# Kernel tuning notes

Measured on AMD Instinct MI355X. Metric: run time of the kernel, lower is better.

Reference implementation:

```python
import jax, jax.numpy as jnp
import numpy as np

S, B, C, H = 384, 2, 768, 12
CC = C // H

def setup_inputs() -> dict:
    key = jax.random.key(0)
    ks = jax.random.split(key, 8)
    x = jax.random.normal(ks[0], (S, B, C), dtype=jnp.float32)
    pe = jax.random.normal(ks[1], (S, S, B, C), dtype=jnp.float32)
    # causal mask: True where key index t > query index s (masked out)
    cm = (jnp.arange(S)[None, :] > jnp.arange(S)[:, None])[:, :, None]
    cm = jnp.broadcast_to(cm, (S, S, B))
    pm = jnp.zeros((S, S, B), dtype=bool)  # unused by the module's forward
    stdv = 1.0 / C ** 0.5
    qkv_w = jax.random.normal(ks[2], (3 * C, C), dtype=jnp.float32) * stdv
    qkv_b = jax.random.normal(ks[3], (3 * C,), dtype=jnp.float32) * stdv
    u = jax.random.uniform(ks[4], (C,), minval=-stdv, maxval=stdv, dtype=jnp.float32)
    w = jax.random.uniform(ks[5], (C,), minval=-stdv, maxval=stdv, dtype=jnp.float32)
    out_w = jax.random.normal(ks[6], (C, C), dtype=jnp.float32) * stdv
    out_b = jax.random.normal(ks[7], (C,), dtype=jnp.float32) * stdv
    return {"x": x, "pe": pe, "cm": cm, "pm": pm, "qkv_w": qkv_w,
            "qkv_b": qkv_b, "u": u, "w": w, "out_w": out_w, "out_b": out_b}

def reference(x, pe, cm, pm, qkv_w, qkv_b, u, w, out_w, out_b):
    s, b, c = x.shape
    qkv = x @ qkv_w.T + qkv_b                       # (s,b,3c)
    q, k, v = jnp.split(qkv, 3, axis=-1)
    q = q.reshape(s, b, H, CC)
    k = k.reshape(s, b, H, CC)
    v = v.reshape(s, b, H, CC)
    uh = u.reshape(1, 1, H, CC)
    wh = w.reshape(1, 1, H, CC)
    # content-content scores with global content bias u
    dd_ud = jnp.einsum('sbhc,tbhc->stbh', q + uh, k)
    # content-position scores against dense pairwise pe
    pe5 = pe.reshape(s, s, b, H, CC)
    dp_wp = jnp.einsum('sbhc,stbhc->stbh', q + wh, pe5)
    scale = 1.0 / CC ** 0.5
    a = (dd_ud + dp_wp) * scale
    a = jnp.where(cm[..., None], -jnp.inf, a)       # causal mask (intended)
    p = jax.nn.softmax(a, axis=1)                   # softmax over key axis t
    o = jnp.einsum('stbh,tbhc->sbhc', p, v).reshape(s, b, c)
    return o @ out_w.T + out_b
```

## Files before the change

kernel.cpp:

```cpp
#include <hip/hip_runtime.h>
#include <hip/hip_bf16.h>
#include <cstdint>

constexpr int kS  = 384;
constexpr int kB  = 2;
constexpr int kC  = 768;
constexpr int kH  = 12;
constexpr int kCC = 64;
constexpr int kHPB = 4;

typedef __attribute__((ext_vector_type(8))) short short8;
typedef __attribute__((ext_vector_type(4))) float f32x4;
typedef __attribute__((ext_vector_type(4))) unsigned short u16x4;
typedef const __attribute__((address_space(1))) unsigned int glb_u32_t;
typedef __attribute__((address_space(3))) unsigned int lds_u32_t;

static __device__ __forceinline__ ushort f2bf(float f) {
  __hip_bfloat16 h = __float2bfloat16(f);
  return *reinterpret_cast<ushort*>(&h);
}

__global__ __launch_bounds__(256) void convert_bf16(
    const float* __restrict__ x, const float* __restrict__ qw,
    const float* __restrict__ ow, ushort* __restrict__ xb,
    ushort* __restrict__ qwb, ushort* __restrict__ owb) {
  int idx = blockIdx.x * 256 + threadIdx.x;
  const float* src;
  ushort* dst;
  if (idx < 147456) {
    src = x; dst = xb;
  } else if (idx < 147456 + 442368) {
    idx -= 147456; src = qw; dst = qwb;
  } else {
    idx -= 589824; src = ow; dst = owb;
  }
  f32x4 v = *reinterpret_cast<const f32x4*>(src + (size_t)idx * 4);
  u16x4 o;
  o[0] = f2bf(v[0]); o[1] = f2bf(v[1]); o[2] = f2bf(v[2]); o[3] = f2bf(v[3]);
  *reinterpret_cast<u16x4*>(dst + (size_t)idx * 4) = o;
}

__global__ __launch_bounds__(256) void gemm_bf16_lds(
    const ushort* __restrict__ Abf, const ushort* __restrict__ Wbf,
    const float* __restrict__ bias, float* __restrict__ Cg,
    int M, int N, int K) {
  __shared__ ushort As[64 * 64];
  __shared__ ushort Ws[64 * 64];
  const int tid = threadIdx.x;
  const int m0 = blockIdx.y * 64, n0 = blockIdx.x * 64;
  const int wv = tid >> 6, l = tid & 63;
  const int wr = wv >> 1, wc = wv & 1;
  const int lr = l & 15, lk = l >> 4;

  f32x4 acc[2][2] = {{{0.f, 0.f, 0.f, 0.f}, {0.f, 0.f, 0.f, 0.f}},
                     {{0.f, 0.f, 0.f, 0.f}, {0.f, 0.f, 0.f, 0.f}}};

  for (int k0 = 0; k0 < K; k0 += 64) {
    __syncthreads();
#pragma unroll
    for (int j = 0; j < 2; ++j) {
      int cid = (j * 4 + wv) * 64 + l;
      int r = cid >> 3, c = cid & 7;
      int cs = c ^ (r & 7);
      const ushort* ga = Abf + (size_t)(m0 + r) * K + k0 + cs * 8;
      __builtin_amdgcn_global_load_lds((glb_u32_t*)ga,
                                       (lds_u32_t*)&As[(cid & ~63) * 8],
                                       16, 0, 0);
      const ushort* gw = Wbf + (size_t)(n0 + r) * K + k0 + cs * 8;
      __builtin_amdgcn_global_load_lds((glb_u32_t*)gw,
                                       (lds_u32_t*)&Ws[(cid & ~63) * 8],
                                       16, 0, 0);
    }
    __syncthreads();
#pragma unroll
    for (int ks = 0; ks < 2; ++ks) {
      short8 af[2], bw[2];
#pragma unroll
      for (int f = 0; f < 2; ++f) {
        int ra = wr * 32 + f * 16 + lr;
        int ca = (ks * 4 + lk) ^ (ra & 7);
        af[f] = *reinterpret_cast<const short8*>(&As[(ra * 8 + ca) * 8]);
        int rb = wc * 32 + f * 16 + lr;
        int cb = (ks * 4 + lk) ^ (rb & 7);
        bw[f] = *reinterpret_cast<const short8*>(&Ws[(rb * 8 + cb) * 8]);
      }
#pragma unroll
      for (int fr = 0; fr < 2; ++fr)
#pragma unroll
        for (int fc = 0; fc < 2; ++fc)
          acc[fr][fc] = __builtin_amdgcn_mfma_f32_16x16x32_bf16(
              af[fr], bw[fc], acc[fr][fc], 0, 0, 0);
    }
  }

#pragma unroll
  for (int fr = 0; fr < 2; ++fr)
#pragma unroll
    for (int fc = 0; fc < 2; ++fc)
#pragma unroll
      for (int j = 0; j < 4; ++j) {
        int m = m0 + wr * 32 + fr * 16 + lk * 4 + j;
        int n = n0 + wc * 32 + fc * 16 + lr;
        Cg[(size_t)m * N + n] = acc[fr][fc][j] + bias[n];
      }
}

__global__ __launch_bounds__(256, 6) void attn_kernel(
    const float* __restrict__ qkv, const float* __restrict__ pe,
    const float* __restrict__ u, const float* __restrict__ w,
    ushort* __restrict__ obf) {
  __shared__ float sc[kHPB][kS];

  const int bid = blockIdx.x;
  const int sb = bid / (kH / kHPB);
  const int hg = bid % (kH / kHPB);
  const int s = kS - 1 - (sb >> 1);
  const int b = sb & 1;
  const int wave = threadIdx.x >> 6;
  const int h = hg * kHPB + wave;
  const int lane = threadIdx.x & 63;
  const int tq = lane >> 4;
  const int cq = (lane & 15) * 4;
  const int ch = h * kCC + cq;
  const float scale = 0.125f;

  const int row = s * kB + b;
  const float4 q4 = *(const float4*)&qkv[(int64_t)row * 3 * kC + ch];
  const float4 u4 = *(const float4*)&u[ch];
  const float4 w4 = *(const float4*)&w[ch];
  float4 qu, qw;
  qu.x = q4.x + u4.x; qu.y = q4.y + u4.y; qu.z = q4.z + u4.z; qu.w = q4.w + u4.w;
  qw.x = q4.x + w4.x; qw.y = q4.y + w4.y; qw.z = q4.z + w4.z; qw.w = q4.w + w4.w;

  const float* kbase = qkv + (int64_t)b * 3 * kC + kC + ch;
  const float* vbase = qkv + (int64_t)b * 3 * kC + 2 * kC + ch;
  const float* pbase = pe + ((int64_t)s * kS * kB + b) * kC + ch;
  const int kstride = kB * 3 * kC;
  const int pstride = kB * kC;

  const int nfull = (s + 1) & ~15;

  int t0 = 0;
  for (; t0 < nfull; t0 += 16) {
    float4 k4[4];
    f32x4 p4[4];
#pragma unroll
    for (int i = 0; i < 4; ++i) {
      int t = t0 + i * 4 + tq;
      k4[i] = *(const float4*)&kbase[(int64_t)t * kstride];
      p4[i] = __builtin_nontemporal_load(
          (const f32x4*)&pbase[(int64_t)t * pstride]);
    }
#pragma unroll
    for (int i = 0; i < 4; ++i) {
      float r = qu.x * k4[i].x + qu.y * k4[i].y + qu.z * k4[i].z +
                qu.w * k4[i].w + qw.x * p4[i][0] + qw.y * p4[i][1] +
                qw.z * p4[i][2] + qw.w * p4[i][3];
      r += __shfl_xor(r, 1);
      r += __shfl_xor(r, 2);
      r += __shfl_xor(r, 4);
      r += __shfl_xor(r, 8);
      if ((lane & 15) == 0) sc[wave][t0 + i * 4 + tq] = r * scale;
    }
  }
  for (; t0 <= s; t0 += 4) {
    int t = t0 + tq;
    int tc = (t <= s) ? t : s;
    float4 k4 = *(const float4*)&kbase[(int64_t)tc * kstride];
    float4 p4 = *(const float4*)&pbase[(int64_t)tc * pstride];
    float r = qu.x * k4.x + qu.y * k4.y + qu.z * k4.z + qu.w * k4.w +
              qw.x * p4.x + qw.y * p4.y + qw.z * p4.z + qw.w * p4.w;
    r += __shfl_xor(r, 1);
    r += __shfl_xor(r, 2);
    r += __shfl_xor(r, 4);
    r += __shfl_xor(r, 8);
    if ((lane & 15) == 0 && t <= s) sc[wave][t] = r * scale;
  }
  __syncthreads();

  float mx = -1e30f;
  for (int t = lane; t <= s; t += 64) mx = fmaxf(mx, sc[wave][t]);
#pragma unroll
  for (int off = 32; off; off >>= 1) mx = fmaxf(mx, __shfl_xor(mx, off, 64));
  float sum = 0.f;
  for (int t = lane; t <= s; t += 64) {
    float e = __expf(sc[wave][t] - mx);
    sc[wave][t] = e;
    sum += e;
  }
#pragma unroll
  for (int off = 32; off; off >>= 1) sum += __shfl_xor(sum, off, 64);
  const float rden = 1.0f / sum;

  float4 oa = {0.f, 0.f, 0.f, 0.f};
  t0 = 0;
  for (; t0 < nfull; t0 += 16) {
    float4 v4[4];
    float p[4];
#pragma unroll
    for (int i = 0; i < 4; ++i) {
      int t = t0 + i * 4 + tq;
      v4[i] = *(const float4*)&vbase[(int64_t)t * kstride];
      p[i] = sc[wave][t];
    }
#pragma unroll
    for (int i = 0; i < 4; ++i) {
      oa.x += p[i] * v4[i].x; oa.y += p[i] * v4[i].y;
      oa.z += p[i] * v4[i].z; oa.w += p[i] * v4[i].w;
    }
  }
  for (; t0 <= s; t0 += 4) {
    int t = t0 + tq;
    if (t <= s) {
      float p = sc[wave][t];
      float4 v4 = *(const float4*)&vbase[(int64_t)t * kstride];
      oa.x += p * v4.x; oa.y += p * v4.y; oa.z += p * v4.z; oa.w += p * v4.w;
    }
  }
#pragma unroll
  for (int off = 16; off <= 32; off <<= 1) {
    oa.x += __shfl_xor(oa.x, off);
    oa.y += __shfl_xor(oa.y, off);
    oa.z += __shfl_xor(oa.z, off);
    oa.w += __shfl_xor(oa.w, off);
  }
  if (lane < 16) {
    u16x4 res;
    res[0] = f2bf(oa.x * rden); res[1] = f2bf(oa.y * rden);
    res[2] = f2bf(oa.z * rden); res[3] = f2bf(oa.w * rden);
    *reinterpret_cast<u16x4*>(&obf[(int64_t)row * kC + ch]) = res;
  }
}

extern "C" void kernel_launch(void* const* d_in, const int* in_sizes, int n_in,
                              void* d_out, int out_size, void* d_ws,
                              size_t ws_size, hipStream_t stream) {
  const float* x     = (const float*)d_in[0];
  const float* pe    = (const float*)d_in[1];
  const float* qkv_w = (const float*)d_in[4];
  const float* qkv_b = (const float*)d_in[5];
  const float* u     = (const float*)d_in[6];
  const float* w     = (const float*)d_in[7];
  const float* out_w = (const float*)d_in[8];
  const float* out_b = (const float*)d_in[9];
  float* out = (float*)d_out;

  char* wsb = (char*)d_ws;
  float*  qkv  = (float*)wsb;
  ushort* xb   = (ushort*)(wsb + 7077888);
  ushort* qwb  = (ushort*)(wsb + 8257536);
  ushort* owb  = (ushort*)(wsb + 11796480);
  ushort* obf  = (ushort*)(wsb + 12976128);

  convert_bf16<<<2880, 256, 0, stream>>>(x, qkv_w, out_w, xb, qwb, owb);

  gemm_bf16_lds<<<dim3(3 * kC / 64, kS * kB / 64), 256, 0, stream>>>(
      xb, qwb, qkv_b, qkv, kS * kB, 3 * kC, kC);

  attn_kernel<<<kS * kB * (kH / kHPB), kHPB * 64, 0, stream>>>(
      qkv, pe, u, w, obf);

  gemm_bf16_lds<<<dim3(kC / 64, kS * kB / 64), 256, 0, stream>>>(
      obf, owb, out_b, out, kS * kB, kC, kC);
}
```

Before: 137.2 us.

## Double-buffer GEMM LDS tiles and drop nontemporal pe loads in attention

The GEMM now double-buffers its A and W tiles in LDS, prefetching the next K-slice with global_load_lds while MFMAs run on the current one. It synchronises with a waitcnt plus barrier instead of two syncthreads per iteration. The attention kernel switches pe loads from nontemporal to regular loads, issues them before the k loads, and moves to ext_vector types. The dominant cost is the pe stream in attention, so the GEMM pipelining only touches a smaller part of the runtime, and dropping the nontemporal hint may change cache behaviour.

```diff
diff --git a/kernel.cpp b/kernel.cpp
--- a/kernel.cpp
+++ b/kernel.cpp
@@ -44,8 +44,8 @@
     const ushort* __restrict__ Abf, const ushort* __restrict__ Wbf,
     const float* __restrict__ bias, float* __restrict__ Cg,
     int M, int N, int K) {
-  __shared__ ushort As[64 * 64];
-  __shared__ ushort Ws[64 * 64];
+  __shared__ ushort As[2][64 * 64];
+  __shared__ ushort Ws[2][64 * 64];
   const int tid = threadIdx.x;
   const int m0 = blockIdx.y * 64, n0 = blockIdx.x * 64;
   const int wv = tid >> 6, l = tid & 63;
@@ -55,23 +55,29 @@
   f32x4 acc[2][2] = {{{0.f, 0.f, 0.f, 0.f}, {0.f, 0.f, 0.f, 0.f}},
                      {{0.f, 0.f, 0.f, 0.f}, {0.f, 0.f, 0.f, 0.f}}};
 
-  for (int k0 = 0; k0 < K; k0 += 64) {
-    __syncthreads();
-#pragma unroll
-    for (int j = 0; j < 2; ++j) {
-      int cid = (j * 4 + wv) * 64 + l;
-      int r = cid >> 3, c = cid & 7;
-      int cs = c ^ (r & 7);
-      const ushort* ga = Abf + (size_t)(m0 + r) * K + k0 + cs * 8;
-      __builtin_amdgcn_global_load_lds((glb_u32_t*)ga,
-                                       (lds_u32_t*)&As[(cid & ~63) * 8],
-                                       16, 0, 0);
-      const ushort* gw = Wbf + (size_t)(n0 + r) * K + k0 + cs * 8;
-      __builtin_amdgcn_global_load_lds((glb_u32_t*)gw,
-                                       (lds_u32_t*)&Ws[(cid & ~63) * 8],
-                                       16, 0, 0);
-    }
-    __syncthreads();
+#define STAGE(buf, k0)                                                        \
+  {                                                                           \
+    _Pragma("unroll") for (int j = 0; j < 2; ++j) {                           \
+      int cid = (j * 4 + wv) * 64 + l;                                        \
+      int r = cid >> 3, c = cid & 7;                                          \
+      int cs = c ^ (r & 7);                                                   \
+      __builtin_amdgcn_global_load_lds(                                       \
+          (glb_u32_t*)(Abf + (size_t)(m0 + r) * K + (k0) + cs * 8),           \
+          (lds_u32_t*)&As[buf][(cid & ~63) * 8], 16, 0, 0);                   \
+      __builtin_amdgcn_global_load_lds(                                       \
+          (glb_u32_t*)(Wbf + (size_t)(n0 + r) * K + (k0) + cs * 8),           \
+          (lds_u32_t*)&Ws[buf][(cid & ~63) * 8], 16, 0, 0);                   \
+    }                                                                         \
+  }
+
+  const int NK = K >> 6;
+  STAGE(0, 0);
+  asm volatile("s_waitcnt vmcnt(0)" ::: "memory");
+  __builtin_amdgcn_s_barrier();
+
+  for (int kt = 0; kt < NK; ++kt) {
+    const int cur = kt & 1;
+    if (kt + 1 < NK) STAGE(cur ^ 1, (kt + 1) * 64);
 #pragma unroll
     for (int ks = 0; ks < 2; ++ks) {
       short8 af[2], bw[2];
@@ -79,10 +85,10 @@
       for (int f = 0; f < 2; ++f) {
         int ra = wr * 32 + f * 16 + lr;
         int ca = (ks * 4 + lk) ^ (ra & 7);
-        af[f] = *reinterpret_cast<const short8*>(&As[(ra * 8 + ca) * 8]);
+        af[f] = *reinterpret_cast<const short8*>(&As[cur][(ra * 8 + ca) * 8]);
         int rb = wc * 32 + f * 16 + lr;
         int cb = (ks * 4 + lk) ^ (rb & 7);
-        bw[f] = *reinterpret_cast<const short8*>(&Ws[(rb * 8 + cb) * 8]);
+        bw[f] = *reinterpret_cast<const short8*>(&Ws[cur][(rb * 8 + cb) * 8]);
       }
 #pragma unroll
       for (int fr = 0; fr < 2; ++fr)
@@ -91,7 +97,10 @@
           acc[fr][fc] = __builtin_amdgcn_mfma_f32_16x16x32_bf16(
               af[fr], bw[fc], acc[fr][fc], 0, 0, 0);
     }
-  }
+    asm volatile("s_waitcnt vmcnt(0)" ::: "memory");
+    __builtin_amdgcn_s_barrier();
+  }
+#undef STAGE
 
 #pragma unroll
   for (int fr = 0; fr < 2; ++fr)
@@ -125,12 +134,11 @@
   const float scale = 0.125f;
 
   const int row = s * kB + b;
-  const float4 q4 = *(const float4*)&qkv[(int64_t)row * 3 * kC + ch];
-  const float4 u4 = *(const float4*)&u[ch];
-  const float4 w4 = *(const float4*)&w[ch];
-  float4 qu, qw;
-  qu.x = q4.x + u4.x; qu.y = q4.y + u4.y; qu.z = q4.z + u4.z; qu.w = q4.w + u4.w;
-  qw.x = q4.x + w4.x; qw.y = q4.y + w4.y; qw.z = q4.z + w4.z; qw.w = q4.w + w4.w;
+  const f32x4 q4 = *(const f32x4*)&qkv[(int64_t)row * 3 * kC + ch];
+  const f32x4 u4 = *(const f32x4*)&u[ch];
+  const f32x4 w4 = *(const f32x4*)&w[ch];
+  const f32x4 qu = q4 + u4;
+  const f32x4 qw = q4 + w4;
 
   const float* kbase = qkv + (int64_t)b * 3 * kC + kC + ch;
   const float* vbase = qkv + (int64_t)b * 3 * kC + 2 * kC + ch;
@@ -142,20 +150,22 @@
 
   int t0 = 0;
   for (; t0 < nfull; t0 += 16) {
-    float4 k4[4];
-    f32x4 p4[4];
+    f32x4 k4[4], p4[4];
 #pragma unroll
     for (int i = 0; i < 4; ++i) {
       int t = t0 + i * 4 + tq;
-      k4[i] = *(const float4*)&kbase[(int64_t)t * kstride];
-      p4[i] = __builtin_nontemporal_load(
-          (const f32x4*)&pbase[(int64_t)t * pstride]);
-    }
-#pragma unroll
-    for (int i = 0; i < 4; ++i) {
-      float r = qu.x * k4[i].x + qu.y * k4[i].y + qu.z * k4[i].z +
-                qu.w * k4[i].w + qw.x * p4[i][0] + qw.y * p4[i][1] +
-                qw.z * p4[i][2] + qw.w * p4[i][3];
+      p4[i] = *(const f32x4*)&pbase[(int64_t)t * pstride];
+    }
+#pragma unroll
+    for (int i = 0; i < 4; ++i) {
+      int t = t0 + i * 4 + tq;
+      k4[i] = *(const f32x4*)&kbase[(int64_t)t * kstride];
+    }
+#pragma unroll
+    for (int i = 0; i < 4; ++i) {
+      float r = qu[0] * k4[i][0] + qu[1] * k4[i][1] + qu[2] * k4[i][2] +
+                qu[3] * k4[i][3] + qw[0] * p4[i][0] + qw[1] * p4[i][1] +
+                qw[2] * p4[i][2] + qw[3] * p4[i][3];
       r += __shfl_xor(r, 1);
       r += __shfl_xor(r, 2);
       r += __shfl_xor(r, 4);
@@ -166,10 +176,10 @@
   for (; t0 <= s; t0 += 4) {
     int t = t0 + tq;
     int tc = (t <= s) ? t : s;
-    float4 k4 = *(const float4*)&kbase[(int64_t)tc * kstride];
-    float4 p4 = *(const float4*)&pbase[(int64_t)tc * pstride];
-    float r = qu.x * k4.x + qu.y * k4.y + qu.z * k4.z + qu.w * k4.w +
-              qw.x * p4.x + qw.y * p4.y + qw.z * p4.z + qw.w * p4.w;
+    f32x4 k4 = *(const f32x4*)&kbase[(int64_t)tc * kstride];
+    f32x4 p4 = *(const f32x4*)&pbase[(int64_t)tc * pstride];
+    float r = qu[0] * k4[0] + qu[1] * k4[1] + qu[2] * k4[2] + qu[3] * k4[3] +
+              qw[0] * p4[0] + qw[1] * p4[1] + qw[2] * p4[2] + qw[3] * p4[3];
     r += __shfl_xor(r, 1);
     r += __shfl_xor(r, 2);
     r += __shfl_xor(r, 4);
@@ -192,42 +202,43 @@
   for (int off = 32; off; off >>= 1) sum += __shfl_xor(sum, off, 64);
   const float rden = 1.0f / sum;
 
-  float4 oa = {0.f, 0.f, 0.f, 0.f};
+  f32x4 oa = {0.f, 0.f, 0.f, 0.f};
   t0 = 0;
   for (; t0 < nfull; t0 += 16) {
-    float4 v4[4];
+    f32x4 v4[4];
     float p[4];
 #pragma unroll
     for (int i = 0; i < 4; ++i) {
       int t = t0 + i * 4 + tq;
-      v4[i] = *(const float4*)&vbase[(int64_t)t * kstride];
+      v4[i] = *(const f32x4*)&vbase[(int64_t)t * kstride];
       p[i] = sc[wave][t];
     }
 #pragma unroll
     for (int i = 0; i < 4; ++i) {
-      oa.x += p[i] * v4[i].x; oa.y += p[i] * v4[i].y;
-      oa.z += p[i] * v4[i].z; oa.w += p[i] * v4[i].w;
+      oa[0] += p[i] * v4[i][0]; oa[1] += p[i] * v4[i][1];
+      oa[2] += p[i] * v4[i][2]; oa[3] += p[i] * v4[i][3];
     }
   }
   for (; t0 <= s; t0 += 4) {
     int t = t0 + tq;
     if (t <= s) {
       float p = sc[wave][t];
-      float4 v4 = *(const float4*)&vbase[(int64_t)t * kstride];
-      oa.x += p * v4.x; oa.y += p * v4.y; oa.z += p * v4.z; oa.w += p * v4.w;
+      f32x4 v4 = *(const f32x4*)&vbase[(int64_t)t * kstride];
+      oa[0] += p * v4[0]; oa[1] += p * v4[1];
+      oa[2] += p * v4[2]; oa[3] += p * v4[3];
     }
   }
 #pragma unroll
   for (int off = 16; off <= 32; off <<= 1) {
-    oa.x += __shfl_xor(oa.x, off);
-    oa.y += __shfl_xor(oa.y, off);
-    oa.z += __shfl_xor(oa.z, off);
-    oa.w += __shfl_xor(oa.w, off);
+    oa[0] += __shfl_xor(oa[0], off);
+    oa[1] += __shfl_xor(oa[1], off);
+    oa[2] += __shfl_xor(oa[2], off);
+    oa[3] += __shfl_xor(oa[3], off);
   }
   if (lane < 16) {
     u16x4 res;
-    res[0] = f2bf(oa.x * rden); res[1] = f2bf(oa.y * rden);
-    res[2] = f2bf(oa.z * rden); res[3] = f2bf(oa.w * rden);
+    res[0] = f2bf(oa[0] * rden); res[1] = f2bf(oa[1] * rden);
+    res[2] = f2bf(oa[2] * rden); res[3] = f2bf(oa[3] * rden);
     *reinterpret_cast<u16x4*>(&obf[(int64_t)row * kC + ch]) = res;
   }
 }
```

After: 149.3 us. 1.09x slower.
